# Performance work log

Hardware: AMD Instinct MI355X
Metric: run time of the kernel (lower is better)

Reference implementation:

```python
import jax, jax.numpy as jnp
import numpy as np

B, T, IN, H = 64, 128, 64, 256  # batch, seq_len, input_size, hidden_size
G = 4 * H                        # gate dim


def setup_inputs() -> dict:
    key = jax.random.key(0)
    ks = jax.random.split(key, 8)
    f32 = jnp.float32

    def p(k, shape, scale=0.05):
        return (jax.random.normal(k, shape, dtype=f32) * scale)

    # forget-gate bias initialized to 1.0 (slice [H:2H]) as in the torch module
    b_mu = jnp.zeros((G,), f32).at[H:2 * H].set(1.0)
    lv = lambda shape: jnp.full(shape, -3.0, f32)  # logvar init = -3.0

    return {
        "x": jax.random.normal(ks[0], (B, T, IN), dtype=f32),
        # layer 0
        "w_ih_mu0": p(ks[1], (G, IN)),
        "w_ih_lv0": lv((G, IN)),
        "w_hh_mu0": p(ks[2], (G, H)),
        "w_hh_lv0": lv((G, H)),
        "b_ih_mu0": b_mu,
        "b_ih_lv0": lv((G,)),
        "b_hh_mu0": jnp.zeros((G,), f32),
        "b_hh_lv0": lv((G,)),
        # layer 1 (input size = H since unidirectional)
        "w_ih_mu1": p(ks[3], (G, H)),
        "w_ih_lv1": lv((G, H)),
        "w_hh_mu1": p(ks[4], (G, H)),
        "w_hh_lv1": lv((G, H)),
        "b_ih_mu1": b_mu,
        "b_ih_lv1": lv((G,)),
        "b_hh_mu1": jnp.zeros((G,), f32),
        "b_hh_lv1": lv((G,)),
    }


def _sample(mu, logvar, k):
    # reparameterization: mu + exp(0.5*logvar) * eps, fresh eps every call (every timestep)
    return mu + jnp.exp(0.5 * logvar) * jax.random.normal(k, mu.shape, mu.dtype)


def _lstm_layer(x_seq, wih_mu, wih_lv, whh_mu, whh_lv,
                bih_mu, bih_lv, bhh_mu, bhh_lv, layer_key):
    # x_seq: (T, B, in) -> (hs (T,B,H), h_T (B,H), c_T (B,H))
    Tn, Bn = x_seq.shape[0], x_seq.shape[1]
    Hn = whh_mu.shape[1]
    keys = jax.random.split(layer_key, Tn)
    h0 = jnp.zeros((Bn, Hn), x_seq.dtype)
    c0 = jnp.zeros((Bn, Hn), x_seq.dtype)

    def step(carry, inp):
        h, c = carry
        x_t, k = inp
        k1, k2, k3, k4 = jax.random.split(k, 4)
        wih = _sample(wih_mu, wih_lv, k1)
        whh = _sample(whh_mu, whh_lv, k2)
        bih = _sample(bih_mu, bih_lv, k3)
        bhh = _sample(bhh_mu, bhh_lv, k4)
        gates = x_t @ wih.T + bih + h @ whh.T + bhh  # (B, 4H)
        i, f, g, o = jnp.split(gates, 4, axis=-1)
        c = jax.nn.sigmoid(f) * c + jax.nn.sigmoid(i) * jnp.tanh(g)
        h = jax.nn.sigmoid(o) * jnp.tanh(c)
        return (h, c), h

    (hT, cT), hs = jax.lax.scan(step, (h0, c0), (x_seq, keys))
    return hs, hT, cT


def reference(x,
              w_ih_mu0, w_ih_lv0, w_hh_mu0, w_hh_lv0,
              b_ih_mu0, b_ih_lv0, b_hh_mu0, b_hh_lv0,
              w_ih_mu1, w_ih_lv1, w_hh_mu1, w_hh_lv1,
              b_ih_mu1, b_ih_lv1, b_hh_mu1, b_hh_lv1):
    base = jax.random.key(42)
    x_seq = jnp.transpose(x, (1, 0, 2))  # batch_first -> (T, B, IN)
    hs0, h0T, c0T = _lstm_layer(x_seq, w_ih_mu0, w_ih_lv0, w_hh_mu0, w_hh_lv0,
                                b_ih_mu0, b_ih_lv0, b_hh_mu0, b_hh_lv0,
                                jax.random.fold_in(base, 0))
    hs1, h1T, c1T = _lstm_layer(hs0, w_ih_mu1, w_ih_lv1, w_hh_mu1, w_hh_lv1,
                                b_ih_mu1, b_ih_lv1, b_hh_mu1, b_hh_lv1,
                                jax.random.fold_in(base, 1))
    output = jnp.transpose(hs1, (1, 0, 2))  # (B, T, H)
    h_n = jnp.stack([h0T, h1T])  # (num_layers, B, H)
    c_n = jnp.stack([c0T, c1T])
    return output, h_n, c_n
```

## Files before the change

### kernel.cpp

```cpp
#include <hip/hip_runtime.h>
#include <stdint.h>


typedef unsigned int u32;
typedef float f32x4 __attribute__((ext_vector_type(4)));

#define Bn 64
#define Tn 128
#define INn 64
#define Hn 256
#define Gn 1024
#define BH (Bn * Hn)

#define OFF_ELV_WIH0 0
#define OFF_ELV_WHH0 65536
#define OFF_ELV_WIH1 327680
#define OFF_ELV_WHH1 589824
#define OFF_ELV_B    851968
#define OFF_H0T      856064
#define OFF_H1T      (OFF_H0T + 2 * Hn * Bn)
#define OFF_KEYS     (OFF_H1T + 2 * Hn * Bn)
#define OFF_BAR      (OFF_KEYS + 2 * Tn * 8)
#define WS_FLOATS    (OFF_BAR + 64)
#define OUT_HN       (Bn * Tn * Hn)

struct KP { u32 a, b; };

__device__ __forceinline__ void st_coh(float* p, float v) {
  __hip_atomic_store(p, v, __ATOMIC_RELAXED, __HIP_MEMORY_SCOPE_AGENT);
}
__device__ __forceinline__ u32 ld_flag(const u32* p) {
  return __hip_atomic_load(p, __ATOMIC_RELAXED, __HIP_MEMORY_SCOPE_AGENT);
}
__device__ __forceinline__ void st_flag(u32* p, u32 v) {
  __hip_atomic_store(p, v, __ATOMIC_RELAXED, __HIP_MEMORY_SCOPE_AGENT);
}

__device__ __forceinline__ KP tf(u32 k0, u32 k1, u32 x0, u32 x1) {
  u32 ks2 = k0 ^ k1 ^ 0x1BD11BDAu;
  x0 += k0; x1 += k1;
#define TFR(r) { x0 += x1; x1 = (x1 << (r)) | (x1 >> (32 - (r))); x1 ^= x0; }
  TFR(13) TFR(15) TFR(26) TFR(6)
  x0 += k1;  x1 += ks2 + 1u;
  TFR(17) TFR(29) TFR(16) TFR(24)
  x0 += ks2; x1 += k0 + 2u;
  TFR(13) TFR(15) TFR(26) TFR(6)
  x0 += k0;  x1 += k1 + 3u;
  TFR(17) TFR(29) TFR(16) TFR(24)
  x0 += k1;  x1 += ks2 + 4u;
  TFR(13) TFR(15) TFR(26) TFR(6)
  x0 += ks2; x1 += k0 + 5u;
#undef TFR
  KP o; o.a = x0; o.b = x1; return o;
}

__device__ __forceinline__ float n01(u32 bits) {
  float f = __uint_as_float((bits >> 9) | 0x3f800000u) - 1.0f;
  float u = fmaxf(-0.99999994f, f * 2.0f - 0.99999994f);
  float w = -log1pf(-u * u);
  float p;
  if (w < 5.0f) {
    float z = w - 2.5f;
    p = 2.81022636e-08f;
    p = 3.43273939e-07f  + p * z;
    p = -3.5233877e-06f  + p * z;
    p = -4.39150654e-06f + p * z;
    p = 0.00021858087f   + p * z;
    p = -0.00125372503f  + p * z;
    p = -0.00417768164f  + p * z;
    p = 0.246640727f     + p * z;
    p = 1.50140941f      + p * z;
  } else {
    float z = sqrtf(w) - 3.0f;
    p = -0.000200214257f;
    p = 0.000100950558f  + p * z;
    p = 0.00134934322f   + p * z;
    p = -0.00367342844f  + p * z;
    p = 0.00573950773f   + p * z;
    p = -0.0076224613f   + p * z;
    p = 0.00943887047f   + p * z;
    p = 1.00167406f      + p * z;
    p = 2.83297682f      + p * z;
  }
  return 1.41421356237f * (p * u);
}

#define POOL_BYTES 51360
#define WBUF_OFF   0
#define INB_OFF    16512
#define BIAS_OFF   51328

template<int LAYER>
__device__ __forceinline__ void sample_weights(
    const float* __restrict__ wihmu, const float* __restrict__ whhmu,
    const float* __restrict__ bihmu, const float* __restrict__ bhhmu,
    const float* __restrict__ ws, float* __restrict__ wbuf,
    float* __restrict__ bias2, int ts, int j0, int tid)
{
  constexpr int Kin  = LAYER ? Hn : INn;
  constexpr int Ktot = Kin + Hn;
  if (ts >= Tn) return;
  const u32* kp = (const u32*)(ws + OFF_KEYS) + (LAYER * Tn + ts) * 8;
  const float* elv_ih  = ws + (LAYER ? OFF_ELV_WIH1 : OFF_ELV_WIH0);
  const float* elv_hh  = ws + (LAYER ? OFF_ELV_WHH1 : OFF_ELV_WHH0);
  const float* belv_ih = ws + OFF_ELV_B + LAYER * 2048;
  const float* belv_hh = belv_ih + 1024;

  const int k = tid;
  if (k < Ktot) {
    bool iswih = k < Kin;
    u32 ka = iswih ? kp[0] : kp[2], kb = iswih ? kp[1] : kp[3];
    const float* mup  = iswih ? wihmu  : whhmu;
    const float* elvp = iswih ? elv_ih : elv_hh;
    int kk = iswih ? k : k - Kin;
    int kstride = iswih ? Kin : Hn;
    #pragma unroll
    for (int gi = 0; gi < 8; ++gi) {
      int g = (gi & 3) * Hn + j0 + (gi >> 2);
      int i = g * kstride + kk;
      KP r = tf(ka, kb, 0u, (u32)i);
      wbuf[gi * 516 + k] = mup[i] + elvp[i] * n01(r.a ^ r.b);
    }
  }
  if (tid < 8) {
    int g = (tid & 3) * Hn + j0 + (tid >> 2);
    KP rb = tf(kp[4], kp[5], 0u, (u32)g);
    KP rh = tf(kp[6], kp[7], 0u, (u32)g);
    bias2[tid] = bihmu[g] + belv_ih[g] * n01(rb.a ^ rb.b)
               + bhhmu[g] + belv_hh[g] * n01(rh.a ^ rh.b);
  }
}

template<int LAYER>
__device__ void step_body(
    const float* x,
    float* ws, float* out, int t, char* pool,
    float& creg, u32* bar)
{
  constexpr int Kin  = LAYER ? Hn : INn;
  constexpr int Ktot = Kin + Hn;
  constexpr int nch  = Ktot / 64;
  const int tid = threadIdx.x;
  const int j0  = (blockIdx.x & 127) * 2;
  const int ts  = LAYER ? (t - 1) : t;

  float* wbuf  = (float*)(pool + WBUF_OFF);
  float* inb   = (float*)(pool + INB_OFF);
  float* gpart = (float*)(pool + INB_OFF);
  float* bias2 = (float*)(pool + BIAS_OFF);

  const float* hT_self = ws + (LAYER ? OFF_H1T : OFF_H0T) + (ts & 1) * (Hn * Bn);
  const float* hT_in   = ws + OFF_H0T + ((ts + 1) & 1) * (Hn * Bn);

  f32x4 pf0[2], pf1[2], pf2[2], pf3[2];
  auto issue = [&](int c, f32x4* pf) {
    #pragma unroll
    for (int m = 0; m < 2; ++m) {
      int f = tid + 512 * m;
      if (LAYER == 0 && c == 0) {
        int b = f >> 4, q4 = (f & 15) * 4;
        const float* p = x + (b * Tn + ts) * INn + q4;
        asm volatile("global_load_dwordx4 %0, %1, off"
                     : "=v"(pf[m]) : "v"(p) : "memory");
      } else {
        int k = f >> 4, b0 = (f & 15) * 4;
        const float* p;
        if (LAYER == 0)      p = hT_self + (c * 64 + k - 64) * Bn + b0;
        else if (c < 4)      p = hT_in   + (c * 64 + k) * Bn + b0;
        else                 p = hT_self + (c * 64 + k - 256) * Bn + b0;
        asm volatile("global_load_dwordx4 %0, %1, off sc1"
                     : "=v"(pf[m]) : "v"(p) : "memory");
      }
    }
  };
  auto pfsel = [&](int c) -> f32x4* {
    switch (c & 3) {
      case 0: return pf0;
      case 1: return pf1;
      case 2: return pf2;
      default: return pf3;
    }
  };
  auto writeb = [&](int c, f32x4* pf) {
    #pragma unroll
    for (int m = 0; m < 2; ++m) {
      int f = tid + 512 * m;
      if (LAYER == 0 && c == 0) {
        int b = f >> 4, seg = f & 15;
        int col = 4 * (seg ^ ((b >> 3) & 7));
        *(f32x4*)&inb[(((c & 1) << 6) + b) * 68 + col] = pf[m];
      } else {
        int k = f >> 4, b0 = (f & 15) * 4;
        int q = k >> 2, kr = k & 3;
        int base = (c & 1) << 6;
        #pragma unroll
        for (int i = 0; i < 4; ++i) {
          int b = b0 + i;
          inb[(base + b) * 68 + 4 * (q ^ ((b >> 3) & 7)) + kr] = pf[m][i];
        }
      }
    }
  };

  issue(0, pf0); issue(1, pf1); issue(2, pf2); issue(3, pf3);
  asm volatile("s_waitcnt vmcnt(6)" ::: "memory");
  __builtin_amdgcn_sched_barrier(0);
  writeb(0, pf0);
  __syncthreads();

  const int kq    = tid >> 5;
  const int bp    = (tid >> 2) & 7;
  const int rhalf = (tid >> 1) & 1;
  const int jj    = tid & 1;
  const int colq  = 4 * (kq ^ bp);

  float acc[4][4];
  #pragma unroll
  for (int r = 0; r < 4; ++r)
    acc[r][0] = acc[r][1] = acc[r][2] = acc[r][3] = 0.f;

  #pragma unroll
  for (int c = 0; c < nch; ++c) {
    if (c + 4 < nch) issue(c + 4, pfsel(c + 4));
    float4 w4[4];
    #pragma unroll
    for (int s = 0; s < 4; ++s)
      w4[s] = *(const float4*)&wbuf[(jj * 4 + s) * 516 + c * 64 + kq * 4];
    #pragma unroll
    for (int rr = 0; rr < 4; ++rr) {
      int b = bp * 8 + rhalf * 4 + rr;
      float4 in4 = *(const float4*)&inb[(((c & 1) << 6) + b) * 68 + colq];
      #pragma unroll
      for (int s = 0; s < 4; ++s)
        acc[rr][s] += in4.x * w4[s].x + in4.y * w4[s].y
                    + in4.z * w4[s].z + in4.w * w4[s].w;
    }
    if (c + 1 < nch) {
      constexpr int last = nch - 1;
      const int hi = (c + 4 < last) ? (c + 4) : last;
      const int rem = hi - (c + 1);
      if (rem >= 3)      asm volatile("s_waitcnt vmcnt(6)" ::: "memory");
      else if (rem == 2) asm volatile("s_waitcnt vmcnt(4)" ::: "memory");
      else if (rem == 1) asm volatile("s_waitcnt vmcnt(2)" ::: "memory");
      else               asm volatile("s_waitcnt vmcnt(0)" ::: "memory");
      __builtin_amdgcn_sched_barrier(0);
      writeb(c + 1, pfsel(c + 1));
    }
    __syncthreads();
  }

  if (LAYER == 0) {
    if (tid == 0) {
      while (ld_flag(bar + 32) < (u32)(128 * t))
        __builtin_amdgcn_s_sleep(2);
    }
    asm volatile("" ::: "memory");
  }

  #pragma unroll
  for (int rr = 0; rr < 4; ++rr) {
    int r = rhalf * 4 + rr;
    float4 v = {acc[rr][0], acc[rr][1], acc[rr][2], acc[rr][3]};
    int col4 = (bp * 16 + r * 2 + jj) ^ bp;
    *(float4*)&gpart[kq * 520 + col4 * 4] = v;
  }
  __syncthreads();

  if (tid < 128) {
    const int b = tid >> 1, j2 = tid & 1;
    const int rbp = b >> 3, rr = b & 7;
    const int col4 = (rbp * 16 + rr * 2 + j2) ^ rbp;
    float4 gq = {0.f, 0.f, 0.f, 0.f};
    #pragma unroll
    for (int q = 0; q < 16; ++q) {
      float4 p = *(const float4*)&gpart[q * 520 + col4 * 4];
      gq.x += p.x; gq.y += p.y; gq.z += p.z; gq.w += p.w;
    }
    const int j = j0 + j2;
    float gI = gq.x + bias2[j2 * 4 + 0];
    float gF = gq.y + bias2[j2 * 4 + 1];
    float gG = gq.z + bias2[j2 * 4 + 2];
    float gO = gq.w + bias2[j2 * 4 + 3];

    float cp = creg;
    float si = 1.f / (1.f + expf(-gI));
    float sf = 1.f / (1.f + expf(-gF));
    float so = 1.f / (1.f + expf(-gO));
    float cn = sf * cp + si * tanhf(gG);
    float hn = so * tanhf(cn);
    creg = cn;
    float* hTn = ws + (LAYER ? OFF_H1T : OFF_H0T) + ((ts + 1) & 1) * (Hn * Bn);
    st_coh(hTn + j * Bn + b, hn);
    if (LAYER == 0) {
      if (ts == Tn - 1) {
        out[OUT_HN + b * Hn + j] = hn;
        out[OUT_HN + 2 * BH + b * Hn + j] = cn;
      }
    } else {
      out[b * (Tn * Hn) + ts * Hn + j] = hn;
      if (ts == Tn - 1) {
        out[OUT_HN + BH + b * Hn + j] = hn;
        out[OUT_HN + 3 * BH + b * Hn + j] = cn;
      }
    }
  }
}

__global__ __launch_bounds__(512) void bayes_lstm_persist(
    const float* __restrict__ x,
    const float* __restrict__ wihmu0, const float* __restrict__ whhmu0,
    const float* __restrict__ bihmu0, const float* __restrict__ bhhmu0,
    const float* __restrict__ wihmu1, const float* __restrict__ whhmu1,
    const float* __restrict__ bihmu1, const float* __restrict__ bhhmu1,
    float* __restrict__ ws, float* __restrict__ out)
{
  __shared__ __align__(16) char pool[POOL_BYTES];
  const int tid = threadIdx.x, bid = blockIdx.x;
  const int layer = bid >> 7, j0 = (bid & 127) * 2;
  float* wbuf  = (float*)(pool + WBUF_OFF);
  float* bias2 = (float*)(pool + BIAS_OFF);
  u32* bar = (u32*)(ws + OFF_BAR);
  u32* cnt_mine = bar + (bid >> 7) * 32;
  float creg = 0.f;

  if (layer == 0)
    sample_weights<0>(wihmu0, whhmu0, bihmu0, bhhmu0, ws, wbuf, bias2, 0, j0, tid);
  __syncthreads();

  for (int t = 0; t <= Tn; ++t) {
    if (layer == 0) {
      if (t < Tn) step_body<0>(x, ws, out, t, pool, creg, bar);
    } else {
      if (t >= 1) step_body<1>(x, ws, out, t, pool, creg, bar);
    }
    if (t == Tn) break;

    __syncthreads();
    if (tid == 0)
      __hip_atomic_fetch_add(cnt_mine, 1u, __ATOMIC_RELAXED,
                             __HIP_MEMORY_SCOPE_AGENT);

    if (layer == 0)
      sample_weights<0>(wihmu0, whhmu0, bihmu0, bhhmu0, ws, wbuf, bias2,
                        t + 1, j0, tid);
    else
      sample_weights<1>(wihmu1, whhmu1, bihmu1, bhhmu1, ws, wbuf, bias2,
                        t, j0, tid);

    if (tid == 0) {
      const u32 tgt = (u32)(128 * (t + 1));
      while (ld_flag(cnt_mine) < tgt)
        __builtin_amdgcn_s_sleep(2);
      if (layer == 1) {
        while (ld_flag(bar) < tgt)
          __builtin_amdgcn_s_sleep(2);
      }
    }
    asm volatile("" ::: "memory");
    __syncthreads();
  }
}

__global__ __launch_bounds__(256) void bayes_lstm_prologue(
    const float* __restrict__ wihlv0, const float* __restrict__ whhlv0,
    const float* __restrict__ bihlv0, const float* __restrict__ bhhlv0,
    const float* __restrict__ wihlv1, const float* __restrict__ whhlv1,
    const float* __restrict__ bihlv1, const float* __restrict__ bhhlv1,
    float* __restrict__ ws)
{
  const int gt = blockIdx.x * 256 + threadIdx.x;
  const int stride = gridDim.x * 256;
  for (int i = gt; i < 65536; i += stride)
    ws[OFF_ELV_WIH0 + i] = expf(0.5f * wihlv0[i]);
  for (int i = gt; i < 262144; i += stride) {
    ws[OFF_ELV_WHH0 + i] = expf(0.5f * whhlv0[i]);
    ws[OFF_ELV_WIH1 + i] = expf(0.5f * wihlv1[i]);
    ws[OFF_ELV_WHH1 + i] = expf(0.5f * whhlv1[i]);
  }
  for (int i = gt; i < 1024; i += stride) {
    ws[OFF_ELV_B + i]        = expf(0.5f * bihlv0[i]);
    ws[OFF_ELV_B + 1024 + i] = expf(0.5f * bhhlv0[i]);
    ws[OFF_ELV_B + 2048 + i] = expf(0.5f * bihlv1[i]);
    ws[OFF_ELV_B + 3072 + i] = expf(0.5f * bhhlv1[i]);
  }
  for (int i = gt; i < 4 * Hn * Bn; i += stride)
    st_coh(ws + OFF_H0T + i, 0.f);
  if (gt < 64)
    st_flag((u32*)(ws + OFF_BAR) + gt, 0u);
  if (gt < 2 * Tn) {
    int l = gt >> 7, ts = gt & 127;
    KP lk  = tf(0u, 42u, 0u, (u32)l);
    KP kt  = tf(lk.a, lk.b, 0u, (u32)ts);
    KP kw  = tf(kt.a, kt.b, 0u, 0u);
    KP ku  = tf(kt.a, kt.b, 0u, 1u);
    KP kbi = tf(kt.a, kt.b, 0u, 2u);
    KP kbh = tf(kt.a, kt.b, 0u, 3u);
    u32* kp = (u32*)(ws + OFF_KEYS) + gt * 8;
    kp[0] = kw.a;  kp[1] = kw.b;  kp[2] = ku.a;  kp[3] = ku.b;
    kp[4] = kbi.a; kp[5] = kbi.b; kp[6] = kbh.a; kp[7] = kbh.b;
  }
}

extern "C" void kernel_launch(void* const* d_in, const int* in_sizes, int n_in,
                              void* d_out, int out_size, void* d_ws, size_t ws_size,
                              hipStream_t stream) {
  (void)in_sizes; (void)n_in; (void)out_size;
  if (ws_size < (size_t)WS_FLOATS * sizeof(float)) return;

  const float* x      = (const float*)d_in[0];
  const float* wihmu0 = (const float*)d_in[1];
  const float* wihlv0 = (const float*)d_in[2];
  const float* whhmu0 = (const float*)d_in[3];
  const float* whhlv0 = (const float*)d_in[4];
  const float* bihmu0 = (const float*)d_in[5];
  const float* bihlv0 = (const float*)d_in[6];
  const float* bhhmu0 = (const float*)d_in[7];
  const float* bhhlv0 = (const float*)d_in[8];
  const float* wihmu1 = (const float*)d_in[9];
  const float* wihlv1 = (const float*)d_in[10];
  const float* whhmu1 = (const float*)d_in[11];
  const float* whhlv1 = (const float*)d_in[12];
  const float* bihmu1 = (const float*)d_in[13];
  const float* bihlv1 = (const float*)d_in[14];
  const float* bhhmu1 = (const float*)d_in[15];
  const float* bhhlv1 = (const float*)d_in[16];
  float* ws  = (float*)d_ws;
  float* out = (float*)d_out;

  bayes_lstm_prologue<<<dim3(256), dim3(256), 0, stream>>>(
      wihlv0, whhlv0, bihlv0, bhhlv0, wihlv1, whhlv1, bihlv1, bhhlv1, ws);

  bayes_lstm_persist<<<dim3(256), dim3(512), 0, stream>>>(
      x, wihmu0, whhmu0, bihmu0, bhhmu0,
      wihmu1, whhmu1, bihmu1, bhhmu1, ws, out);
}
```

Measured before the change: 2.163 ms.

## Double-buffer sampled weights and overlap next-step sampling with current matvec

Sampled weights and biases are now double-buffered in shared memory, so sampling for the next timestep is interleaved chunk by chunk into the current step's matvec loop instead of running as a separate phase between steps. Inputs are now loaded from global memory straight into registers in the layout each thread consumes, which removes the LDS staging buffer and the per-chunk syncthreads. The cross-k reduction is partly done with a wavefront shuffle before writing partial sums, which halves the gpart reduction. The cost is more registers held for prefetch and extra sampling work inside the critical path of each step.

```diff
diff --git a/kernel.cpp b/kernel.cpp
--- a/kernel.cpp
+++ b/kernel.cpp
@@ -9,7 +9,6 @@
 #define Tn 128
 #define INn 64
 #define Hn 256
-#define Gn 1024
 #define BH (Bn * Hn)
 
 #define OFF_ELV_WIH0 0
@@ -85,17 +84,17 @@
   return 1.41421356237f * (p * u);
 }
 
-#define POOL_BYTES 51360
+#define POOL_BYTES 49600
 #define WBUF_OFF   0
-#define INB_OFF    16512
-#define BIAS_OFF   51328
+#define WSTRIDE    (8 * 516)
+#define GPART_OFF  33024
+#define BIAS_OFF   49536
 
 template<int LAYER>
-__device__ __forceinline__ void sample_weights(
-    const float* __restrict__ wihmu, const float* __restrict__ whhmu,
-    const float* __restrict__ bihmu, const float* __restrict__ bhhmu,
-    const float* __restrict__ ws, float* __restrict__ wbuf,
-    float* __restrict__ bias2, int ts, int j0, int tid)
+__device__ __forceinline__ void sample_full(
+    const float* wihmu, const float* whhmu,
+    const float* bihmu, const float* bhhmu,
+    const float* ws, float* wbufN, float* bias2N, int ts, int j0, int tid)
 {
   constexpr int Kin  = LAYER ? Hn : INn;
   constexpr int Ktot = Kin + Hn;
@@ -105,7 +104,6 @@
   const float* elv_hh  = ws + (LAYER ? OFF_ELV_WHH1 : OFF_ELV_WHH0);
   const float* belv_ih = ws + OFF_ELV_B + LAYER * 2048;
   const float* belv_hh = belv_ih + 1024;
-
   const int k = tid;
   if (k < Ktot) {
     bool iswih = k < Kin;
@@ -119,23 +117,24 @@
       int g = (gi & 3) * Hn + j0 + (gi >> 2);
       int i = g * kstride + kk;
       KP r = tf(ka, kb, 0u, (u32)i);
-      wbuf[gi * 516 + k] = mup[i] + elvp[i] * n01(r.a ^ r.b);
+      wbufN[gi * 516 + k] = mup[i] + elvp[i] * n01(r.a ^ r.b);
     }
   }
   if (tid < 8) {
     int g = (tid & 3) * Hn + j0 + (tid >> 2);
     KP rb = tf(kp[4], kp[5], 0u, (u32)g);
     KP rh = tf(kp[6], kp[7], 0u, (u32)g);
-    bias2[tid] = bihmu[g] + belv_ih[g] * n01(rb.a ^ rb.b)
-               + bhhmu[g] + belv_hh[g] * n01(rh.a ^ rh.b);
+    bias2N[tid] = bihmu[g] + belv_ih[g] * n01(rb.a ^ rb.b)
+                + bhhmu[g] + belv_hh[g] * n01(rh.a ^ rh.b);
   }
 }
 
 template<int LAYER>
 __device__ void step_body(
-    const float* x,
-    float* ws, float* out, int t, char* pool,
-    float& creg, u32* bar)
+    const float* x, float* ws, float* out, int t, char* pool,
+    float& creg, u32* bar,
+    const float* wihmu, const float* whhmu,
+    const float* bihmu, const float* bhhmu)
 {
   constexpr int Kin  = LAYER ? Hn : INn;
   constexpr int Ktot = Kin + Hn;
@@ -143,144 +142,175 @@
   const int tid = threadIdx.x;
   const int j0  = (blockIdx.x & 127) * 2;
   const int ts  = LAYER ? (t - 1) : t;
-
-  float* wbuf  = (float*)(pool + WBUF_OFF);
-  float* inb   = (float*)(pool + INB_OFF);
-  float* gpart = (float*)(pool + INB_OFF);
-  float* bias2 = (float*)(pool + BIAS_OFF);
+  const bool act = LAYER ? (t >= 1) : (t < Tn);
+
+  float* wbufC  = (float*)(pool + WBUF_OFF) + (t & 1) * WSTRIDE;
+  float* wbufN  = (float*)(pool + WBUF_OFF) + ((t + 1) & 1) * WSTRIDE;
+  float* gpart  = (float*)(pool + GPART_OFF);
+  float* bias2C = (float*)(pool + BIAS_OFF) + (t & 1) * 8;
+  float* bias2N = (float*)(pool + BIAS_OFF) + ((t + 1) & 1) * 8;
+
+  const int nts = LAYER ? t : t + 1;
+  const bool dosample = nts < Tn;
+  const u32* kp = (const u32*)(ws + OFF_KEYS)
+                  + (LAYER * Tn + (dosample ? nts : 0)) * 8;
+  const float* elv_ih  = ws + (LAYER ? OFF_ELV_WIH1 : OFF_ELV_WIH0);
+  const float* elv_hh  = ws + (LAYER ? OFF_ELV_WHH1 : OFF_ELV_WHH0);
+  const bool iswih = tid < Kin;
+  const u32 ka = iswih ? kp[0] : kp[2], kb2 = iswih ? kp[1] : kp[3];
+  const float* mup  = iswih ? wihmu  : whhmu;
+  const float* elvp = iswih ? elv_ih : elv_hh;
+  const int kk_ = iswih ? tid : tid - Kin;
+  const int kstride = iswih ? Kin : Hn;
+  const bool samp_ok = dosample && (tid < Ktot);
+
+  auto do_eval = [&](int gi) {
+    int g = (gi & 3) * Hn + j0 + (gi >> 2);
+    int i = g * kstride + kk_;
+    KP r = tf(ka, kb2, 0u, (u32)i);
+    wbufN[gi * 516 + tid] = mup[i] + elvp[i] * n01(r.a ^ r.b);
+  };
+  if (dosample && tid < 8) {
+    const float* belv_ih = ws + OFF_ELV_B + LAYER * 2048;
+    const float* belv_hh = belv_ih + 1024;
+    int g = (tid & 3) * Hn + j0 + (tid >> 2);
+    KP rb = tf(kp[4], kp[5], 0u, (u32)g);
+    KP rh = tf(kp[6], kp[7], 0u, (u32)g);
+    bias2N[tid] = bihmu[g] + belv_ih[g] * n01(rb.a ^ rb.b)
+                + bhhmu[g] + belv_hh[g] * n01(rh.a ^ rh.b);
+  }
 
   const float* hT_self = ws + (LAYER ? OFF_H1T : OFF_H0T) + (ts & 1) * (Hn * Bn);
   const float* hT_in   = ws + OFF_H0T + ((ts + 1) & 1) * (Hn * Bn);
 
-  f32x4 pf0[2], pf1[2], pf2[2], pf3[2];
-  auto issue = [&](int c, f32x4* pf) {
-    #pragma unroll
-    for (int m = 0; m < 2; ++m) {
-      int f = tid + 512 * m;
-      if (LAYER == 0 && c == 0) {
-        int b = f >> 4, q4 = (f & 15) * 4;
-        const float* p = x + (b * Tn + ts) * INn + q4;
-        asm volatile("global_load_dwordx4 %0, %1, off"
-                     : "=v"(pf[m]) : "v"(p) : "memory");
-      } else {
-        int k = f >> 4, b0 = (f & 15) * 4;
-        const float* p;
-        if (LAYER == 0)      p = hT_self + (c * 64 + k - 64) * Bn + b0;
-        else if (c < 4)      p = hT_in   + (c * 64 + k) * Bn + b0;
-        else                 p = hT_self + (c * 64 + k - 256) * Bn + b0;
-        asm volatile("global_load_dwordx4 %0, %1, off sc1"
-                     : "=v"(pf[m]) : "v"(p) : "memory");
-      }
-    }
-  };
-  auto pfsel = [&](int c) -> f32x4* {
-    switch (c & 3) {
-      case 0: return pf0;
-      case 1: return pf1;
-      case 2: return pf2;
-      default: return pf3;
-    }
-  };
-  auto writeb = [&](int c, f32x4* pf) {
-    #pragma unroll
-    for (int m = 0; m < 2; ++m) {
-      int f = tid + 512 * m;
-      if (LAYER == 0 && c == 0) {
-        int b = f >> 4, seg = f & 15;
-        int col = 4 * (seg ^ ((b >> 3) & 7));
-        *(f32x4*)&inb[(((c & 1) << 6) + b) * 68 + col] = pf[m];
-      } else {
-        int k = f >> 4, b0 = (f & 15) * 4;
-        int q = k >> 2, kr = k & 3;
-        int base = (c & 1) << 6;
-        #pragma unroll
-        for (int i = 0; i < 4; ++i) {
-          int b = b0 + i;
-          inb[(base + b) * 68 + 4 * (q ^ ((b >> 3) & 7)) + kr] = pf[m][i];
-        }
-      }
-    }
-  };
-
-  issue(0, pf0); issue(1, pf1); issue(2, pf2); issue(3, pf3);
-  asm volatile("s_waitcnt vmcnt(6)" ::: "memory");
-  __builtin_amdgcn_sched_barrier(0);
-  writeb(0, pf0);
-  __syncthreads();
-
-  const int kq    = tid >> 5;
-  const int bp    = (tid >> 2) & 7;
-  const int rhalf = (tid >> 1) & 1;
-  const int jj    = tid & 1;
-  const int colq  = 4 * (kq ^ bp);
+  const int kq = tid >> 5, bp = (tid >> 2) & 7, rhalf = (tid >> 1) & 1,
+            jj = tid & 1;
+  const int b0 = bp * 8 + rhalf * 4;
 
   float acc[4][4];
   #pragma unroll
   for (int r = 0; r < 4; ++r)
     acc[r][0] = acc[r][1] = acc[r][2] = acc[r][3] = 0.f;
 
-  #pragma unroll
-  for (int c = 0; c < nch; ++c) {
-    if (c + 4 < nch) issue(c + 4, pfsel(c + 4));
-    float4 w4[4];
+  if (act) {
+    f32x4 pf0[4], pf1[4], pf2[4], pf3[4];
+    auto pfsel = [&](int c) -> f32x4* {
+      switch (c & 3) {
+        case 0: return pf0;
+        case 1: return pf1;
+        case 2: return pf2;
+        default: return pf3;
+      }
+    };
+    auto issue = [&](int c) {
+      f32x4* P = pfsel(c);
+      if (LAYER == 0 && c == 0) {
+        #pragma unroll
+        for (int rr = 0; rr < 4; ++rr) {
+          const float* p = x + ((b0 + rr) * Tn + ts) * INn + kq * 4;
+          asm volatile("global_load_dwordx4 %0, %1, off"
+                       : "=v"(P[rr]) : "v"(p) : "memory");
+        }
+      } else {
+        const float* src; int kb_;
+        if (LAYER == 0)      { src = hT_self; kb_ = (c - 1) * 64 + kq * 4; }
+        else if (c < 4)      { src = hT_in;   kb_ = c * 64 + kq * 4; }
+        else                 { src = hT_self; kb_ = (c - 4) * 64 + kq * 4; }
+        #pragma unroll
+        for (int kk2 = 0; kk2 < 4; ++kk2) {
+          const float* p = src + (kb_ + kk2) * Bn + b0;
+          asm volatile("global_load_dwordx4 %0, %1, off sc1"
+                       : "=v"(P[kk2]) : "v"(p) : "memory");
+        }
+      }
+    };
+
+    issue(0); issue(1); issue(2);
     #pragma unroll
-    for (int s = 0; s < 4; ++s)
-      w4[s] = *(const float4*)&wbuf[(jj * 4 + s) * 516 + c * 64 + kq * 4];
-    #pragma unroll
-    for (int rr = 0; rr < 4; ++rr) {
-      int b = bp * 8 + rhalf * 4 + rr;
-      float4 in4 = *(const float4*)&inb[(((c & 1) << 6) + b) * 68 + colq];
+    for (int c = 0; c < nch; ++c) {
+      if (c + 3 < nch) issue(c + 3);
+      const int rem = (c + 3 < nch) ? 3 : (nch - 1 - c);
+      if (rem >= 3)      asm volatile("s_waitcnt vmcnt(12)" ::: "memory");
+      else if (rem == 2) asm volatile("s_waitcnt vmcnt(8)" ::: "memory");
+      else if (rem == 1) asm volatile("s_waitcnt vmcnt(4)" ::: "memory");
+      else               asm volatile("s_waitcnt vmcnt(0)" ::: "memory");
+      __builtin_amdgcn_sched_barrier(0);
+
+      f32x4* P = pfsel(c);
+      f32x4 w4[4];
       #pragma unroll
       for (int s = 0; s < 4; ++s)
-        acc[rr][s] += in4.x * w4[s].x + in4.y * w4[s].y
-                    + in4.z * w4[s].z + in4.w * w4[s].w;
-    }
-    if (c + 1 < nch) {
-      constexpr int last = nch - 1;
-      const int hi = (c + 4 < last) ? (c + 4) : last;
-      const int rem = hi - (c + 1);
-      if (rem >= 3)      asm volatile("s_waitcnt vmcnt(6)" ::: "memory");
-      else if (rem == 2) asm volatile("s_waitcnt vmcnt(4)" ::: "memory");
-      else if (rem == 1) asm volatile("s_waitcnt vmcnt(2)" ::: "memory");
-      else               asm volatile("s_waitcnt vmcnt(0)" ::: "memory");
-      __builtin_amdgcn_sched_barrier(0);
-      writeb(c + 1, pfsel(c + 1));
-    }
-    __syncthreads();
-  }
-
-  if (LAYER == 0) {
-    if (tid == 0) {
+        w4[s] = *(const f32x4*)&wbufC[(jj * 4 + s) * 516 + c * 64 + kq * 4];
+      if (LAYER == 0 && c == 0) {
+        #pragma unroll
+        for (int rr = 0; rr < 4; ++rr)
+          #pragma unroll
+          for (int s = 0; s < 4; ++s)
+            acc[rr][s] += P[rr][0] * w4[s][0] + P[rr][1] * w4[s][1]
+                        + P[rr][2] * w4[s][2] + P[rr][3] * w4[s][3];
+      } else {
+        #pragma unroll
+        for (int kk2 = 0; kk2 < 4; ++kk2)
+          #pragma unroll
+          for (int rr = 0; rr < 4; ++rr)
+            #pragma unroll
+            for (int s = 0; s < 4; ++s)
+              acc[rr][s] += P[kk2][rr] * w4[s][kk2];
+      }
+
+      if (samp_ok) {
+        const int elo = (c * 8) / nch, ehi = ((c + 1) * 8) / nch;
+        #pragma unroll
+        for (int e = 0; e < 8; ++e)
+          if (e >= elo && e < ehi) do_eval(e);
+      }
+    }
+  } else {
+    if (samp_ok) {
+      #pragma unroll
+      for (int e = 0; e < 8; ++e) do_eval(e);
+    }
+  }
+
+  if (act) {
+    #pragma unroll
+    for (int rr = 0; rr < 4; ++rr)
+      #pragma unroll
+      for (int s = 0; s < 4; ++s)
+        acc[rr][s] += __shfl_xor(acc[rr][s], 32);
+    if ((tid & 32) == 0) {
+      const int w = tid >> 6;
+      #pragma unroll
+      for (int rr = 0; rr < 4; ++rr) {
+        int r = rhalf * 4 + rr;
+        f32x4 v = {acc[rr][0], acc[rr][1], acc[rr][2], acc[rr][3]};
+        int col4 = (bp * 16 + r * 2 + jj) ^ bp;
+        *(f32x4*)&gpart[w * 516 + col4 * 4] = v;
+      }
+    }
+    if (LAYER == 0 && tid == 0) {
       while (ld_flag(bar + 32) < (u32)(128 * t))
         __builtin_amdgcn_s_sleep(2);
     }
     asm volatile("" ::: "memory");
   }
-
-  #pragma unroll
-  for (int rr = 0; rr < 4; ++rr) {
-    int r = rhalf * 4 + rr;
-    float4 v = {acc[rr][0], acc[rr][1], acc[rr][2], acc[rr][3]};
-    int col4 = (bp * 16 + r * 2 + jj) ^ bp;
-    *(float4*)&gpart[kq * 520 + col4 * 4] = v;
-  }
   __syncthreads();
 
-  if (tid < 128) {
+  if (act && tid < 128) {
     const int b = tid >> 1, j2 = tid & 1;
     const int rbp = b >> 3, rr = b & 7;
     const int col4 = (rbp * 16 + rr * 2 + j2) ^ rbp;
-    float4 gq = {0.f, 0.f, 0.f, 0.f};
+    f32x4 gq = {0.f, 0.f, 0.f, 0.f};
     #pragma unroll
-    for (int q = 0; q < 16; ++q) {
-      float4 p = *(const float4*)&gpart[q * 520 + col4 * 4];
+    for (int q = 0; q < 8; ++q) {
+      f32x4 p = *(const f32x4*)&gpart[q * 516 + col4 * 4];
       gq.x += p.x; gq.y += p.y; gq.z += p.z; gq.w += p.w;
     }
     const int j = j0 + j2;
-    float gI = gq.x + bias2[j2 * 4 + 0];
-    float gF = gq.y + bias2[j2 * 4 + 1];
-    float gG = gq.z + bias2[j2 * 4 + 2];
-    float gO = gq.w + bias2[j2 * 4 + 3];
+    float gI = gq.x + bias2C[j2 * 4 + 0];
+    float gF = gq.y + bias2C[j2 * 4 + 1];
+    float gG = gq.z + bias2C[j2 * 4 + 2];
+    float gO = gq.w + bias2C[j2 * 4 + 3];
 
     float cp = creg;
     float si = 1.f / (1.f + expf(-gI));
@@ -304,6 +334,7 @@
       }
     }
   }
+  __syncthreads();
 }
 
 __global__ __launch_bounds__(512) void bayes_lstm_persist(
@@ -317,36 +348,28 @@
   __shared__ __align__(16) char pool[POOL_BYTES];
   const int tid = threadIdx.x, bid = blockIdx.x;
   const int layer = bid >> 7, j0 = (bid & 127) * 2;
-  float* wbuf  = (float*)(pool + WBUF_OFF);
-  float* bias2 = (float*)(pool + BIAS_OFF);
   u32* bar = (u32*)(ws + OFF_BAR);
-  u32* cnt_mine = bar + (bid >> 7) * 32;
+  u32* cnt_mine = bar + layer * 32;
   float creg = 0.f;
 
   if (layer == 0)
-    sample_weights<0>(wihmu0, whhmu0, bihmu0, bhhmu0, ws, wbuf, bias2, 0, j0, tid);
+    sample_full<0>(wihmu0, whhmu0, bihmu0, bhhmu0, ws,
+                   (float*)(pool + WBUF_OFF), (float*)(pool + BIAS_OFF),
+                   0, j0, tid);
   __syncthreads();
 
   for (int t = 0; t <= Tn; ++t) {
-    if (layer == 0) {
-      if (t < Tn) step_body<0>(x, ws, out, t, pool, creg, bar);
-    } else {
-      if (t >= 1) step_body<1>(x, ws, out, t, pool, creg, bar);
-    }
+    if (layer == 0)
+      step_body<0>(x, ws, out, t, pool, creg, bar,
+                   wihmu0, whhmu0, bihmu0, bhhmu0);
+    else
+      step_body<1>(x, ws, out, t, pool, creg, bar,
+                   wihmu1, whhmu1, bihmu1, bhhmu1);
     if (t == Tn) break;
 
-    __syncthreads();
     if (tid == 0)
       __hip_atomic_fetch_add(cnt_mine, 1u, __ATOMIC_RELAXED,
                              __HIP_MEMORY_SCOPE_AGENT);
-
-    if (layer == 0)
-      sample_weights<0>(wihmu0, whhmu0, bihmu0, bhhmu0, ws, wbuf, bias2,
-                        t + 1, j0, tid);
-    else
-      sample_weights<1>(wihmu1, whhmu1, bihmu1, bhhmu1, ws, wbuf, bias2,
-                        t, j0, tid);
-
     if (tid == 0) {
       const u32 tgt = (u32)(128 * (t + 1));
       while (ld_flag(cnt_mine) < tgt)
```

Measured after the change: 3.699 ms. 1.71x slower.
